# Optimization experiments

Measured on AMD Instinct MI355X. Metric: run time of the kernel, lower is better.

## Reference

```python
import jax, jax.numpy as jnp
import numpy as np

BS, SEQ, D, H = 2, 2048, 1024, 16
HD = D // H  # head_dim = 64


def setup_inputs() -> dict:
    key = jax.random.key(0)
    kx, kw = jax.random.split(key)
    x = jax.random.normal(kx, (BS, SEQ, D), dtype=jnp.float32)
    # qkv Linear: weight [3D, D] (xavier_normal), bias zeros
    std = float(np.sqrt(2.0 / (D + 3 * D)))
    W_qkv = jax.random.normal(kw, (3 * D, D), dtype=jnp.float32) * std
    b_qkv = jnp.zeros((3 * D,), dtype=jnp.float32)
    return {"x": x, "W_qkv": W_qkv, "b_qkv": b_qkv}


def reference(x, W_qkv, b_qkv):
    bs, seq_len, embed_dim = x.shape
    # fused QKV projection: [bs, seq, 3D]
    qkv = x @ W_qkv.T + b_qkv
    qkv = qkv.reshape(bs, seq_len, 3, H, HD)
    qkv = jnp.transpose(qkv, (2, 0, 3, 1, 4))  # [3, bs, H, seq, HD]
    Q, K, V = qkv[0], qkv[1], qkv[2]
    # past_kv is None -> total_len == seq_len, past_len == 0
    scores = jnp.einsum("bhqd,bhkd->bhqk", Q, K) / jnp.sqrt(jnp.float32(HD))
    # causal mask: True above diagonal -> -inf
    mask = jnp.triu(jnp.ones((seq_len, seq_len), dtype=bool), k=1)
    scores = jnp.where(mask[None, None, :, :], -jnp.inf, scores)
    probs = jax.nn.softmax(scores, axis=-1)
    # attn_dropout = 0.0 (eval) -> identity
    out = jnp.einsum("bhqk,bhkd->bhqd", probs, V)
    out = jnp.transpose(out, (0, 2, 1, 3)).reshape(bs, seq_len, embed_dim)
    return (out, (K, V))
```

## Files before the change

kernel.cpp:

```cpp
#include <hip/hip_runtime.h>

typedef __bf16 bf16_t;
typedef __bf16 bf16x8 __attribute__((ext_vector_type(8)));
typedef float f32x4 __attribute__((ext_vector_type(4)));
typedef unsigned long long u64;

__device__ __forceinline__ unsigned short bfbits(float f) {
  unsigned u = __float_as_uint(f);
  u += 0x7fffu + ((u >> 16) & 1u);
  return (unsigned short)(u >> 16);
}
__device__ __forceinline__ bf16_t f2bf(float f) {
  unsigned short s = bfbits(f);
  union { unsigned short s; bf16_t b; } cv; cv.s = s; return cv.b;
}

__device__ __forceinline__ void gl16(const void* g, void* l) {
  __builtin_amdgcn_global_load_lds(
      (const __attribute__((address_space(1))) void*)g,
      (__attribute__((address_space(3))) void*)l,
      16, 0, 0);
}

__global__ __launch_bounds__(256) void cvt_kernel(const float* __restrict__ x,
                                                  const float* __restrict__ Wf,
                                                  bf16_t* __restrict__ xb,
                                                  bf16_t* __restrict__ wb) {
  const int i = blockIdx.x * 256 + threadIdx.x;
  const float* src; bf16_t* dst; int j;
  if (i < 524288) { j = i; src = x; dst = xb; }
  else            { j = i - 524288; src = Wf; dst = wb; }
  const float4* s = (const float4*)src + (size_t)j * 2;
  float4 a = s[0], b = s[1];
  bf16x8 o;
  o[0] = f2bf(a.x); o[1] = f2bf(a.y); o[2] = f2bf(a.z); o[3] = f2bf(a.w);
  o[4] = f2bf(b.x); o[5] = f2bf(b.y); o[6] = f2bf(b.z); o[7] = f2bf(b.w);
  const int row = j >> 7, jr = j & 127;
  const int dstc = (row << 7) + (jr & ~3) + ((jr & 3) ^ ((row >> 1) & 3));
  *((bf16x8*)dst + dstc) = o;
}

#define GEMM_K 1024
__global__ __launch_bounds__(256) void qkv_gemm(
    const bf16_t* __restrict__ A,
    const bf16_t* __restrict__ B,
    const float* __restrict__ bias,
    float* __restrict__ Ko, float* __restrict__ Vo,
    bf16_t* __restrict__ Qb, bf16_t* __restrict__ Kb,
    bf16_t* __restrict__ Vt,
    int* __restrict__ qcnt)
{
  if (blockIdx.x == 0 && threadIdx.x == 0) *qcnt = 0;
  __shared__ bf16_t lsA[3][4096];
  __shared__ bf16_t lsB[3][4096];
  const int tid = threadIdx.x;
  const int lane = tid & 63;
  const int ln = lane & 15, qd = lane >> 4;
  const int wid = tid >> 6;
  const int wm = wid & 1, wn = wid >> 1;
  const int xcd = blockIdx.x & 7;
  const int j = blockIdx.x >> 3;
  const int bn = xcd * 3 + (j % 3);
  const int bm = j / 3;
  const int m0 = bm * 128, n0 = bn * 128;
  const int qs = qd ^ ((ln >> 1) & 3);

  f32x4 acc[4][4] = {};

  const int c0 = tid, c1 = tid + 256;
  const bf16_t* ga0 = A + (size_t)(m0 + (c0 >> 2)) * GEMM_K + (c0 & 3) * 8;
  const bf16_t* ga1 = A + (size_t)(m0 + (c1 >> 2)) * GEMM_K + (c1 & 3) * 8;
  const bf16_t* gb0 = B + (size_t)(n0 + (c0 >> 2)) * GEMM_K + (c0 & 3) * 8;
  const bf16_t* gb1 = B + (size_t)(n0 + (c1 >> 2)) * GEMM_K + (c1 & 3) * 8;

#define STAGE(t, slot)                                   \
  do {                                                   \
    const int ko_ = (t) * 32;                            \
    gl16(ga0 + ko_, &lsA[(slot)][c0 * 8]);               \
    gl16(ga1 + ko_, &lsA[(slot)][c1 * 8]);               \
    gl16(gb0 + ko_, &lsB[(slot)][c0 * 8]);               \
    gl16(gb1 + ko_, &lsB[(slot)][c1 * 8]);               \
  } while (0)

#define COMPUTE(slot)                                                          \
  do {                                                                         \
    bf16x8 af[4], bf[4];                                                       \
    _Pragma("unroll")                                                          \
    for (int mi = 0; mi < 4; ++mi)                                             \
      af[mi] = *(const bf16x8*)&lsA[(slot)][(wm * 64 + mi * 16 + ln) * 32 + qs * 8]; \
    _Pragma("unroll")                                                          \
    for (int ni = 0; ni < 4; ++ni)                                             \
      bf[ni] = *(const bf16x8*)&lsB[(slot)][(wn * 64 + ni * 16 + ln) * 32 + qs * 8]; \
    _Pragma("unroll")                                                          \
    for (int mi = 0; mi < 4; ++mi)                                             \
      _Pragma("unroll")                                                        \
      for (int ni = 0; ni < 4; ++ni)                                           \
        acc[mi][ni] = __builtin_amdgcn_mfma_f32_16x16x32_bf16(af[mi], bf[ni], acc[mi][ni], 0, 0, 0); \
  } while (0)

#define WAITBAR(n)                                        \
  do {                                                    \
    asm volatile("s_waitcnt vmcnt(" #n ")" ::: "memory"); \
    __builtin_amdgcn_s_barrier();                         \
  } while (0)

  STAGE(0, 0);
  STAGE(1, 1);
#pragma unroll
  for (int t = 0; t < 30; ++t) {
    WAITBAR(4);
    STAGE(t + 2, (t + 2) % 3);
    COMPUTE(t % 3);
  }
  WAITBAR(4); COMPUTE(0);
  WAITBAR(0); COMPUTE(1);

#undef STAGE
#undef COMPUTE
#undef WAITBAR

  const int sec = n0 >> 10;
#pragma unroll
  for (int mi = 0; mi < 4; ++mi) {
#pragma unroll
    for (int ni = 0; ni < 4; ++ni) {
      const int colg = n0 + wn * 64 + ni * 16 + ln;
      const float bv = bias[colg];
      const int cc = colg & 1023, h = cc >> 6, hd = cc & 63;
      if (sec == 2) {
        unsigned u[4];
#pragma unroll
        for (int r = 0; r < 4; ++r) {
          const int mg = m0 + wm * 64 + mi * 16 + qd * 4 + r;
          const int b = mg >> 11, s = mg & 2047;
          const float val = acc[mi][ni][r] + bv;
          Vo[((size_t)((b * 16 + h) * 2048 + s)) * 64 + hd] = val;
          u[r] = __float_as_uint(val);
        }
        const int mg0 = m0 + wm * 64 + mi * 16 + qd * 4;
        const int b0 = mg0 >> 11, s0 = mg0 & 2047;
        const unsigned lo = (u[1] & 0xFFFF0000u) | (u[0] >> 16);
        const unsigned hi = (u[3] & 0xFFFF0000u) | (u[2] >> 16);
        const size_t vb = (size_t)(b0 * 16 + h) * 131072 + (size_t)(s0 >> 6) * 4096 +
                          (size_t)hd * 64 + ((((s0 >> 3) & 7) ^ (hd & 7)) << 3) + (s0 & 7);
        *(u64*)&Vt[vb] = ((u64)hi << 32) | lo;
      } else {
#pragma unroll
        for (int r = 0; r < 4; ++r) {
          const int mg = m0 + wm * 64 + mi * 16 + qd * 4 + r;
          const int b = mg >> 11, s = mg & 2047;
          const float val = acc[mi][ni][r] + bv;
          const int bhi = b * 16 + h;
          const size_t sidx = (size_t)bhi * 131072 + (size_t)(s >> 6) * 4096 +
                              (size_t)(s & 63) * 64 + (((hd >> 3) ^ (s & 7)) << 3) + (hd & 7);
          if (sec == 0) {
            Qb[sidx] = f2bf(val * 0.18033688f);
          } else {
            Ko[((size_t)(bhi * 2048 + s)) * 64 + hd] = val;
            Kb[sidx] = f2bf(val);
          }
        }
      }
    }
  }
}

__global__ __launch_bounds__(512, 4) void attn_kernel(
    const bf16_t* __restrict__ Qb,
    const bf16_t* __restrict__ Kb,
    const bf16_t* __restrict__ Vt,
    float* __restrict__ Out,
    int* __restrict__ qcnt)
{
  __shared__ bf16_t lk[2][4096];
  __shared__ bf16_t lv[2][4096];
  __shared__ bf16_t lp[8192];
  __shared__ int task_sh;
  const int tid = threadIdx.x;
  const int lane = tid & 63, ln = lane & 15, qd = lane >> 4;
  const int w = tid >> 6;
  const int l7 = ln & 7;

  for (;;) {
    __syncthreads();
    if (tid == 0) task_sh = atomicAdd(qcnt, 1);
    __syncthreads();
    const int task = task_sh;
    if (task >= 512) break;
    const int it = (task < 256) ? (15 - (task >> 5)) : ((task - 256) >> 5);
    const int bh = task & 31;
    const int b = bh >> 4, h = bh & 15;

    const bf16_t* qbase = Qb + (size_t)bh * 131072 + (size_t)it * 8192;
    const bf16_t* kbase = Kb + (size_t)bh * 131072;
    const bf16_t* vbase = Vt + (size_t)bh * 131072;

    f32x4 oc[4] = {};
    float lsum = 0.f;
    const int qg = it * 128 + w * 16 + ln;
    const int q = w * 16 + ln;
    const int nt = 2 * (it + 1);

#define STG(t, slot)                                              \
    do {                                                          \
      gl16(kbase + (size_t)(t) * 4096 + tid * 8, &lk[(slot)][tid * 8]); \
      gl16(vbase + (size_t)(t) * 4096 + tid * 8, &lv[(slot)][tid * 8]); \
    } while (0)

#define CTILE(kt, slot)                                                        \
    do {                                                                       \
      if (!((kt) == 2 * it + 1 && w < 4)) {                                    \
        const bool diag = ((kt) >= 2 * it);                                    \
        f32x4 sa[4] = {};                                                      \
        _Pragma("unroll")                                                      \
        for (int kk = 0; kk < 2; ++kk) {                                       \
          bf16x8 ak[4];                                                        \
          _Pragma("unroll")                                                    \
          for (int ki = 0; ki < 4; ++ki)                                       \
            ak[ki] = *(const bf16x8*)&lk[(slot)][(ki * 16 + ln) * 64 + (((kk * 4 + qd) ^ l7) << 3)]; \
          _Pragma("unroll")                                                    \
          for (int ki = 0; ki < 4; ++ki)                                       \
            sa[ki] = __builtin_amdgcn_mfma_f32_16x16x32_bf16(ak[ki], afq[kk], sa[ki], 0, 0, 0); \
        }                                                                      \
        _Pragma("unroll")                                                      \
        for (int ki = 0; ki < 4; ++ki) {                                       \
          const int kb0 = (kt) * 64 + ki * 16 + qd * 4;                        \
          float p0 = __builtin_amdgcn_exp2f(sa[ki][0]);                        \
          float p1 = __builtin_amdgcn_exp2f(sa[ki][1]);                        \
          float p2 = __builtin_amdgcn_exp2f(sa[ki][2]);                        \
          float p3 = __builtin_amdgcn_exp2f(sa[ki][3]);                        \
          if (diag) {                                                          \
            if (kb0 + 0 > qg) p0 = 0.f;                                        \
            if (kb0 + 1 > qg) p1 = 0.f;                                        \
            if (kb0 + 2 > qg) p2 = 0.f;                                        \
            if (kb0 + 3 > qg) p3 = 0.f;                                        \
          }                                                                    \
          lsum += (p0 + p1) + (p2 + p3);                                       \
          const unsigned lo = (__float_as_uint(p1) & 0xFFFF0000u) | (__float_as_uint(p0) >> 16); \
          const unsigned hi = (__float_as_uint(p3) & 0xFFFF0000u) | (__float_as_uint(p2) >> 16); \
          const int g = (ki * 2 + (qd >> 1)) ^ l7;                             \
          *(u64*)&lp[q * 64 + g * 8 + (qd & 1) * 4] = ((u64)hi << 32) | lo;    \
        }                                                                      \
        _Pragma("unroll")                                                      \
        for (int kk = 0; kk < 2; ++kk) {                                       \
          bf16x8 afp, bfv[4];                                                  \
          afp = *(const bf16x8*)&lp[q * 64 + (((kk * 4 + qd) ^ l7) << 3)];     \
          _Pragma("unroll")                                                    \
          for (int ni = 0; ni < 4; ++ni)                                       \
            bfv[ni] = *(const bf16x8*)&lv[(slot)][(ni * 16 + ln) * 64 + (((kk * 4 + qd) ^ l7) << 3)]; \
          _Pragma("unroll")                                                    \
          for (int ni = 0; ni < 4; ++ni)                                       \
            oc[ni] = __builtin_amdgcn_mfma_f32_16x16x32_bf16(afp, bfv[ni], oc[ni], 0, 0, 0); \
        }                                                                      \
      }                                                                        \
    } while (0)

#define WB0                                               \
    do {                                                  \
      asm volatile("s_waitcnt vmcnt(0)" ::: "memory");    \
      __builtin_amdgcn_s_barrier();                       \
    } while (0)

    STG(0, 0);
    bf16x8 afq[2];
    {
      const int row = w * 16 + ln;
#pragma unroll
      for (int kk = 0; kk < 2; ++kk)
        afq[kk] = *(const bf16x8*)(qbase + (row >> 6) * 4096 + (row & 63) * 64 +
                                   (((kk * 4 + qd) ^ l7) << 3));
    }
    WB0;

    for (int s = 0; s < nt; s += 2) {
      STG(s + 1, 1);
      CTILE(s, 0);
      WB0;
      if (s + 2 < nt) STG(s + 2, 0);
      CTILE(s + 1, 1);
      WB0;
    }

#undef STG
#undef CTILE
#undef WB0

    float ls = lsum;
    ls += __shfl_xor(ls, 16);
    ls += __shfl_xor(ls, 32);
#pragma unroll
    for (int r = 0; r < 4; ++r) {
      const float lval = __shfl(ls, qd * 4 + r);
      const float inv = 1.0f / lval;
      const int rowq = it * 128 + w * 16 + qd * 4 + r;
#pragma unroll
      for (int ni = 0; ni < 4; ++ni) {
        const int colh = ni * 16 + ln;
        Out[(size_t)(b * 2048 + rowq) * 1024 + h * 64 + colh] = oc[ni][r] * inv;
      }
    }
  }
}

extern "C" void kernel_launch(void* const* d_in, const int* in_sizes, int n_in,
                              void* d_out, int out_size, void* d_ws, size_t ws_size,
                              hipStream_t stream) {
  const float* x = (const float*)d_in[0];
  const float* W = (const float*)d_in[1];
  const float* bq = (const float*)d_in[2];
  float* out = (float*)d_out;
  float* Ko = out + 4194304;
  float* Vo = out + 8388608;
  char* ws = (char*)d_ws;
  bf16_t* xb = (bf16_t*)ws;
  bf16_t* wb = (bf16_t*)(ws + 8388608);
  bf16_t* Qb = (bf16_t*)(ws + 14680064);
  bf16_t* Kb = (bf16_t*)(ws + 23068672);
  bf16_t* Vt = (bf16_t*)(ws + 31457280);
  int*    qcnt = (int*)(ws + 39845888);

  hipLaunchKernelGGL(cvt_kernel, dim3(3584), dim3(256), 0, stream, x, W, xb, wb);
  hipLaunchKernelGGL(qkv_gemm, dim3(768), dim3(256), 0, stream, xb, wb, bq, Ko, Vo, Qb, Kb, Vt, qcnt);
  hipLaunchKernelGGL(attn_kernel, dim3(512), dim3(512), 0, stream, Qb, Kb, Vt, out, qcnt);
}
```

Baseline: 165.9 us.

## Split long causal query tiles along KV into two partial tasks plus combine kernel

Query tiles in the upper half (it>=8) are split into two tasks, one over KV tiles 0-15 and one over the remaining tiles. Each writes an unnormalized partial output and row sum, and a new combine kernel adds them and normalizes. This balances per-task work across the persistent attention blocks so no block is left with a long tail. The cost is an extra kernel launch, an extra fp32 round-trip for half the output, and workspace reuse that overlaps the xb buffer. The split is only correct if the softmax uses a fixed max, which appears to be the case since there is no running-max rescale.

```diff
diff --git a/kernel.cpp b/kernel.cpp
--- a/kernel.cpp
+++ b/kernel.cpp
@@ -170,6 +170,9 @@
     const bf16_t* __restrict__ Kb,
     const bf16_t* __restrict__ Vt,
     float* __restrict__ Out,
+    float* __restrict__ PB,
+    float* __restrict__ LA,
+    float* __restrict__ LB,
     int* __restrict__ qcnt)
 {
   __shared__ bf16_t lk[2][4096];
@@ -186,9 +189,16 @@
     if (tid == 0) task_sh = atomicAdd(qcnt, 1);
     __syncthreads();
     const int task = task_sh;
-    if (task >= 512) break;
-    const int it = (task < 256) ? (15 - (task >> 5)) : ((task - 256) >> 5);
-    const int bh = task & 31;
+    if (task >= 768) break;
+    int bh, it, kt0, ktN, mode;
+    if (task < 256) {
+      bh = task & 31; it = 8 + ((task >> 5) & 7);
+      kt0 = 0; ktN = 16; mode = 1;
+    } else {
+      const int p = task - 256, grp = p >> 6, within = p & 63;
+      if (within < 32) { bh = within;      it = 15 - grp; kt0 = 16; ktN = 2 * (it + 1) - 16; mode = 2; }
+      else             { bh = within - 32; it = 7 - grp;  kt0 = 0;  ktN = 2 * (it + 1);      mode = 0; }
+    }
     const int b = bh >> 4, h = bh & 15;
 
     const bf16_t* qbase = Qb + (size_t)bh * 131072 + (size_t)it * 8192;
@@ -199,7 +209,6 @@
     float lsum = 0.f;
     const int qg = it * 128 + w * 16 + ln;
     const int q = w * 16 + ln;
-    const int nt = 2 * (it + 1);
 
 #define STG(t, slot)                                              \
     do {                                                          \
@@ -261,7 +270,7 @@
       __builtin_amdgcn_s_barrier();                       \
     } while (0)
 
-    STG(0, 0);
+    STG(kt0, 0);
     bf16x8 afq[2];
     {
       const int row = w * 16 + ln;
@@ -272,12 +281,12 @@
     }
     WB0;
 
-    for (int s = 0; s < nt; s += 2) {
-      STG(s + 1, 1);
-      CTILE(s, 0);
+    for (int s = 0; s < ktN; s += 2) {
+      STG(kt0 + s + 1, 1);
+      CTILE(kt0 + s, 0);
       WB0;
-      if (s + 2 < nt) STG(s + 2, 0);
-      CTILE(s + 1, 1);
+      if (s + 2 < ktN) STG(kt0 + s + 2, 0);
+      CTILE(kt0 + s + 1, 1);
       WB0;
     }
 
@@ -291,15 +300,38 @@
 #pragma unroll
     for (int r = 0; r < 4; ++r) {
       const float lval = __shfl(ls, qd * 4 + r);
-      const float inv = 1.0f / lval;
-      const int rowq = it * 128 + w * 16 + qd * 4 + r;
-#pragma unroll
-      for (int ni = 0; ni < 4; ++ni) {
-        const int colh = ni * 16 + ln;
-        Out[(size_t)(b * 2048 + rowq) * 1024 + h * 64 + colh] = oc[ni][r] * inv;
+      const int rowl = w * 16 + qd * 4 + r;
+      const int rowq = it * 128 + rowl;
+      if (mode == 0) {
+        const float inv = 1.0f / lval;
+#pragma unroll
+        for (int ni = 0; ni < 4; ++ni)
+          Out[(size_t)(b * 2048 + rowq) * 1024 + h * 64 + ni * 16 + ln] = oc[ni][r] * inv;
+      } else if (mode == 1) {
+#pragma unroll
+        for (int ni = 0; ni < 4; ++ni)
+          Out[(size_t)(b * 2048 + rowq) * 1024 + h * 64 + ni * 16 + ln] = oc[ni][r];
+        if (ln == 0) LA[bh * 1024 + (it - 8) * 128 + rowl] = lval;
+      } else {
+        const int pr = bh * 1024 + (it - 8) * 128 + rowl;
+#pragma unroll
+        for (int ni = 0; ni < 4; ++ni)
+          PB[(size_t)pr * 64 + ni * 16 + ln] = oc[ni][r];
+        if (ln == 0) LB[pr] = lval;
       }
     }
   }
+}
+
+__global__ __launch_bounds__(256) void combine_kernel(
+    float* __restrict__ Out, const float* __restrict__ PB,
+    const float* __restrict__ LA, const float* __restrict__ LB) {
+  const int e = blockIdx.x * 256 + threadIdx.x;
+  const int bhrow = e >> 6, hd = e & 63;
+  const int bh = bhrow >> 10, rloc = bhrow & 1023;
+  const int b = bh >> 4, h = bh & 15;
+  const size_t oaddr = ((size_t)(b * 2048 + 1024 + rloc)) * 1024 + h * 64 + hd;
+  Out[oaddr] = (Out[oaddr] + PB[e]) / (LA[bhrow] + LB[bhrow]);
 }
 
 extern "C" void kernel_launch(void* const* d_in, const int* in_sizes, int n_in,
@@ -318,8 +350,12 @@
   bf16_t* Kb = (bf16_t*)(ws + 23068672);
   bf16_t* Vt = (bf16_t*)(ws + 31457280);
   int*    qcnt = (int*)(ws + 39845888);
+  float*  PB = (float*)ws;
+  float*  LA = (float*)(ws + 8388608);
+  float*  LB = (float*)(ws + 8519680);
 
   hipLaunchKernelGGL(cvt_kernel, dim3(3584), dim3(256), 0, stream, x, W, xb, wb);
   hipLaunchKernelGGL(qkv_gemm, dim3(768), dim3(256), 0, stream, xb, wb, bq, Ko, Vo, Qb, Kb, Vt, qcnt);
-  hipLaunchKernelGGL(attn_kernel, dim3(512), dim3(512), 0, stream, Qb, Kb, Vt, out, qcnt);
-}
+  hipLaunchKernelGGL(attn_kernel, dim3(512), dim3(512), 0, stream, Qb, Kb, Vt, out, PB, LA, LB, qcnt);
+  hipLaunchKernelGGL(combine_kernel, dim3(8192), dim3(256), 0, stream, out, PB, LA, LB);
+}
```

Result: no change. 167.2 us (+0.8%).
